# Optimization experiments

Measured on AMD Instinct MI355X. Metric: run time of the kernel, lower is better.

Reference implementation:

```python
import jax, jax.numpy as jnp
import numpy as np


def setup_inputs() -> dict:
    key = jax.random.key(0)
    k1, k2, k3, k4 = jax.random.split(key, 4)
    B, OUT, IN, K = 64, 4096, 25088, 32
    x = jax.random.normal(k1, (B, IN), dtype=jnp.float32)
    labels = jax.random.randint(k2, (OUT, IN), 0, K, dtype=jnp.int32)
    centroids = jax.random.normal(k3, (K,), dtype=jnp.float32)
    bias = jax.random.normal(k4, (OUT,), dtype=jnp.float32)
    return {"x": x, "labels": labels, "centroids": centroids, "bias": bias}


def reference(x, labels, centroids, bias):
    # Dequantize: reconstruct weight [OUT, IN] by looking labels up in the codebook
    W = centroids[labels]                      # [OUT, IN] gather
    # addmm(bias, x, W.T): [B, IN] @ [IN, OUT] + [OUT]
    return x @ W.T + bias
```

## Files before the change

### kernel.cpp

```cpp
#include <hip/hip_runtime.h>
#include <stdint.h>

typedef float f32x4 __attribute__((ext_vector_type(4)));
typedef short bf16x8 __attribute__((ext_vector_type(8)));
typedef int   i32x4  __attribute__((ext_vector_type(4)));

#define IN_DIM   25088
#define OUT_DIM  4096
#define BATCH    64
#define SPLITS   28
#define KBLK     64
#define NBLK     14
#define WG_N     128
#define LSTR     72

#define CONV_BLOCKS 784
#define INIT_BLOCKS 64

__device__ __forceinline__ uint32_t f2bf(float f) {
    uint32_t u = __builtin_bit_cast(uint32_t, f);
    return (u + 0x7FFFu + ((u >> 16) & 1u)) >> 16;
}
__device__ __forceinline__ uint32_t pack2(float a, float b) {
    return f2bf(a) | (f2bf(b) << 16);
}

__global__ __launch_bounds__(256) void prep(const float* __restrict__ x,
                                            const float* __restrict__ bias,
                                            uint32_t* __restrict__ xb,
                                            float* __restrict__ out) {
    if (blockIdx.x < CONV_BLOCKS) {
        const size_t i = blockIdx.x * 256 + threadIdx.x;
        const float4 v0 = *(const float4*)(x + i * 8);
        const float4 v1 = *(const float4*)(x + i * 8 + 4);
        uint4 o;
        o.x = pack2(v0.x, v0.y); o.y = pack2(v0.z, v0.w);
        o.z = pack2(v1.x, v1.y); o.w = pack2(v1.z, v1.w);
        *(uint4*)(xb + i * 4) = o;
    } else {
        const size_t g = (size_t)(blockIdx.x - CONV_BLOCKS) * 256 + threadIdx.x;
        const float4* b4 = (const float4*)bias;
        float4* o4 = (float4*)out;
        #pragma unroll
        for (int r = 0; r < 4; ++r) {
            const size_t j = g * 4 + r;
            o4[j] = b4[j & (OUT_DIM / 4 - 1)];
        }
    }
}

__global__ __launch_bounds__(256) void qlinear_main(
    const int*      __restrict__ labels,
    const float*    __restrict__ centroids,
    const uint16_t* __restrict__ xb,
    float*          __restrict__ out)
{
    __shared__ __align__(16) uint32_t table[1024];
    __shared__ __align__(16) uint16_t wt[WG_N * LSTR];
    __shared__ __align__(16) uint16_t xt[BATCH * LSTR];

    const int t     = threadIdx.x;
    const int wgn   = blockIdx.x & 31;
    const int split = blockIdx.x >> 5;
    const int o0    = wgn * WG_N;
    const int kbase = split * (KBLK * NBLK);

    #pragma unroll
    for (int e = 0; e < 4; ++e) {
        const int i = t + 256 * e;
        table[i] = f2bf(centroids[i & 31]) | (f2bf(centroids[i >> 5]) << 16);
    }

    const int lane = t & 63;
    const int wave = t >> 6;
    const int ln   = lane & 15;
    const int lq   = lane >> 4;

    const int srow = t >> 3;
    const int skc  = (t & 7) * 8;

    const int xrow = t >> 2;
    const int xseg = (t & 3) * 16;

    const int* lbase[4];
    #pragma unroll
    for (int p = 0; p < 4; ++p)
        lbase[p] = labels + (size_t)(o0 + p * 32 + srow) * IN_DIM + kbase + skc;

    f32x4 acc[4][2] = {};

    i32x4 pl[4][2];
    #pragma unroll
    for (int p = 0; p < 4; ++p) {
        pl[p][0] = __builtin_nontemporal_load((const i32x4*)lbase[p]);
        pl[p][1] = __builtin_nontemporal_load((const i32x4*)lbase[p] + 1);
    }

    for (int blk = 0; blk < NBLK; ++blk) {
        const int k0 = kbase + blk * KBLK;

        i32x4 npl[4][2];
        if (blk + 1 < NBLK) {
            #pragma unroll
            for (int p = 0; p < 4; ++p) {
                const i32x4* lp = (const i32x4*)(lbase[p] + (blk + 1) * KBLK);
                npl[p][0] = __builtin_nontemporal_load(lp);
                npl[p][1] = __builtin_nontemporal_load(lp + 1);
            }
        }

        __syncthreads();

        #pragma unroll
        for (int p = 0; p < 4; ++p) {
            const int row = p * 32 + srow;
            uint4 w;
            w.x = table[(uint32_t)pl[p][0].x | ((uint32_t)pl[p][0].y << 5)];
            w.y = table[(uint32_t)pl[p][0].z | ((uint32_t)pl[p][0].w << 5)];
            w.z = table[(uint32_t)pl[p][1].x | ((uint32_t)pl[p][1].y << 5)];
            w.w = table[(uint32_t)pl[p][1].z | ((uint32_t)pl[p][1].w << 5)];
            *(uint4*)(wt + row * LSTR + skc) = w;
        }
        {
            const uint16_t* xp = xb + (size_t)xrow * IN_DIM + k0 + xseg;
            const bf16x8 v0 = *(const bf16x8*)xp;
            const bf16x8 v1 = *(const bf16x8*)(xp + 8);
            *(bf16x8*)(xt + xrow * LSTR + xseg)     = v0;
            *(bf16x8*)(xt + xrow * LSTR + xseg + 8) = v1;
        }
        __syncthreads();

        #pragma unroll
        for (int ks = 0; ks < 2; ++ks) {
            const int kk = ks * 32 + lq * 8;
            bf16x8 a[4], b[2];
            #pragma unroll
            for (int mt = 0; mt < 4; ++mt)
                a[mt] = *(const bf16x8*)(xt + (mt * 16 + ln) * LSTR + kk);
            #pragma unroll
            for (int nt = 0; nt < 2; ++nt)
                b[nt] = *(const bf16x8*)(wt + (wave * 32 + nt * 16 + ln) * LSTR + kk);
            #pragma unroll
            for (int mt = 0; mt < 4; ++mt)
                #pragma unroll
                for (int nt = 0; nt < 2; ++nt)
                    acc[mt][nt] = __builtin_amdgcn_mfma_f32_16x16x32_bf16(
                        a[mt], b[nt], acc[mt][nt], 0, 0, 0);
        }

        #pragma unroll
        for (int p = 0; p < 4; ++p) {
            pl[p][0] = npl[p][0];
            pl[p][1] = npl[p][1];
        }
    }

    #pragma unroll
    for (int mt = 0; mt < 4; ++mt)
        #pragma unroll
        for (int nt = 0; nt < 2; ++nt) {
            const int o = o0 + wave * 32 + nt * 16 + ln;
            #pragma unroll
            for (int r = 0; r < 4; ++r)
                atomicAdd(out + (size_t)(mt * 16 + lq * 4 + r) * OUT_DIM + o,
                          acc[mt][nt][r]);
        }
}

extern "C" void kernel_launch(void* const* d_in, const int* in_sizes, int n_in,
                              void* d_out, int out_size, void* d_ws, size_t ws_size,
                              hipStream_t stream) {
    const float* x         = (const float*)d_in[0];
    const int*   labels    = (const int*)d_in[1];
    const float* centroids = (const float*)d_in[2];
    const float* bias      = (const float*)d_in[3];
    float* out = (float*)d_out;

    uint32_t* xb = (uint32_t*)d_ws;

    prep<<<CONV_BLOCKS + INIT_BLOCKS, 256, 0, stream>>>(x, bias, xb, out);
    qlinear_main<<<32 * SPLITS, 256, 0, stream>>>(labels, centroids,
                                                  (const uint16_t*)xb, out);
}
```

Measured before the change: 543.4 us.

## Load labels and x directly into MFMA fragment registers, dropping LDS staging

Each lane now loads the label and bf16 activation data that its MFMA fragments need straight from global memory, and decodes the weights through the shared codebook table in registers. The LDS tiles for W and x and the two barriers per k-block are removed. This cuts LDS traffic and synchronisation. In exchange, the x tile is no longer shared across waves, so each wave re-reads it from global or cache, and the label loads become less coalesced (64-byte chunks per row per lane group).

```diff
diff --git a/kernel.cpp b/kernel.cpp
--- a/kernel.cpp
+++ b/kernel.cpp
@@ -12,7 +12,6 @@
 #define KBLK     64
 #define NBLK     14
 #define WG_N     128
-#define LSTR     72
 
 #define CONV_BLOCKS 784
 #define INIT_BLOCKS 64
@@ -56,8 +55,6 @@
     float*          __restrict__ out)
 {
     __shared__ __align__(16) uint32_t table[1024];
-    __shared__ __align__(16) uint16_t wt[WG_N * LSTR];
-    __shared__ __align__(16) uint16_t xt[BATCH * LSTR];
 
     const int t     = threadIdx.x;
     const int wgn   = blockIdx.x & 31;
@@ -70,88 +67,85 @@
         const int i = t + 256 * e;
         table[i] = f2bf(centroids[i & 31]) | (f2bf(centroids[i >> 5]) << 16);
     }
+    __syncthreads();
 
     const int lane = t & 63;
     const int wave = t >> 6;
     const int ln   = lane & 15;
     const int lq   = lane >> 4;
 
-    const int srow = t >> 3;
-    const int skc  = (t & 7) * 8;
+    const int* lp0 = labels + (size_t)(o0 + wave * 32 +  0 + ln) * IN_DIM + kbase + lq * 8;
+    const int* lp1 = labels + (size_t)(o0 + wave * 32 + 16 + ln) * IN_DIM + kbase + lq * 8;
 
-    const int xrow = t >> 2;
-    const int xseg = (t & 3) * 16;
-
-    const int* lbase[4];
+    const uint16_t* xp[4];
     #pragma unroll
-    for (int p = 0; p < 4; ++p)
-        lbase[p] = labels + (size_t)(o0 + p * 32 + srow) * IN_DIM + kbase + skc;
+    for (int mt = 0; mt < 4; ++mt)
+        xp[mt] = xb + (size_t)(mt * 16 + ln) * IN_DIM + kbase + lq * 8;
 
     f32x4 acc[4][2] = {};
 
-    i32x4 pl[4][2];
+    i32x4 cur[2][2][2];
     #pragma unroll
-    for (int p = 0; p < 4; ++p) {
-        pl[p][0] = __builtin_nontemporal_load((const i32x4*)lbase[p]);
-        pl[p][1] = __builtin_nontemporal_load((const i32x4*)lbase[p] + 1);
+    for (int nt = 0; nt < 2; ++nt) {
+        const int* lp = nt ? lp1 : lp0;
+        #pragma unroll
+        for (int ks = 0; ks < 2; ++ks) {
+            const i32x4* p = (const i32x4*)(lp + ks * 32);
+            cur[nt][ks][0] = __builtin_nontemporal_load(p);
+            cur[nt][ks][1] = __builtin_nontemporal_load(p + 1);
+        }
     }
 
     for (int blk = 0; blk < NBLK; ++blk) {
-        const int k0 = kbase + blk * KBLK;
+        const int koff = blk * KBLK;
 
-        i32x4 npl[4][2];
+        bf16x8 a[2][4];
+        #pragma unroll
+        for (int ks = 0; ks < 2; ++ks)
+            #pragma unroll
+            for (int mt = 0; mt < 4; ++mt)
+                a[ks][mt] = *(const bf16x8*)(xp[mt] + koff + ks * 32);
+
+        i32x4 nxt[2][2][2];
         if (blk + 1 < NBLK) {
             #pragma unroll
-            for (int p = 0; p < 4; ++p) {
-                const i32x4* lp = (const i32x4*)(lbase[p] + (blk + 1) * KBLK);
-                npl[p][0] = __builtin_nontemporal_load(lp);
-                npl[p][1] = __builtin_nontemporal_load(lp + 1);
+            for (int nt = 0; nt < 2; ++nt) {
+                const int* lp = (nt ? lp1 : lp0) + koff + KBLK;
+                #pragma unroll
+                for (int ks = 0; ks < 2; ++ks) {
+                    const i32x4* p = (const i32x4*)(lp + ks * 32);
+                    nxt[nt][ks][0] = __builtin_nontemporal_load(p);
+                    nxt[nt][ks][1] = __builtin_nontemporal_load(p + 1);
+                }
             }
         }
 
-        __syncthreads();
-
-        #pragma unroll
-        for (int p = 0; p < 4; ++p) {
-            const int row = p * 32 + srow;
-            uint4 w;
-            w.x = table[(uint32_t)pl[p][0].x | ((uint32_t)pl[p][0].y << 5)];
-            w.y = table[(uint32_t)pl[p][0].z | ((uint32_t)pl[p][0].w << 5)];
-            w.z = table[(uint32_t)pl[p][1].x | ((uint32_t)pl[p][1].y << 5)];
-            w.w = table[(uint32_t)pl[p][1].z | ((uint32_t)pl[p][1].w << 5)];
-            *(uint4*)(wt + row * LSTR + skc) = w;
-        }
-        {
-            const uint16_t* xp = xb + (size_t)xrow * IN_DIM + k0 + xseg;
-            const bf16x8 v0 = *(const bf16x8*)xp;
-            const bf16x8 v1 = *(const bf16x8*)(xp + 8);
-            *(bf16x8*)(xt + xrow * LSTR + xseg)     = v0;
-            *(bf16x8*)(xt + xrow * LSTR + xseg + 8) = v1;
-        }
-        __syncthreads();
-
         #pragma unroll
         for (int ks = 0; ks < 2; ++ks) {
-            const int kk = ks * 32 + lq * 8;
-            bf16x8 a[4], b[2];
             #pragma unroll
-            for (int mt = 0; mt < 4; ++mt)
-                a[mt] = *(const bf16x8*)(xt + (mt * 16 + ln) * LSTR + kk);
+            for (int nt = 0; nt < 2; ++nt) {
+                union { bf16x8 v; uint32_t u[4]; } b;
+                const i32x4 v0 = cur[nt][ks][0];
+                const i32x4 v1 = cur[nt][ks][1];
+                b.u[0] = table[(uint32_t)v0.x | ((uint32_t)v0.y << 5)];
+                b.u[1] = table[(uint32_t)v0.z | ((uint32_t)v0.w << 5)];
+                b.u[2] = table[(uint32_t)v1.x | ((uint32_t)v1.y << 5)];
+                b.u[3] = table[(uint32_t)v1.z | ((uint32_t)v1.w << 5)];
+                #pragma unroll
+                for (int mt = 0; mt < 4; ++mt)
+                    acc[mt][nt] = __builtin_amdgcn_mfma_f32_16x16x32_bf16(
+                        a[ks][mt], b.v, acc[mt][nt], 0, 0, 0);
+            }
+        }
+
+        if (blk + 1 < NBLK) {
             #pragma unroll
             for (int nt = 0; nt < 2; ++nt)
-                b[nt] = *(const bf16x8*)(wt + (wave * 32 + nt * 16 + ln) * LSTR + kk);
-            #pragma unroll
-            for (int mt = 0; mt < 4; ++mt)
                 #pragma unroll
-                for (int nt = 0; nt < 2; ++nt)
-                    acc[mt][nt] = __builtin_amdgcn_mfma_f32_16x16x32_bf16(
-                        a[mt], b[nt], acc[mt][nt], 0, 0, 0);
-        }
-
-        #pragma unroll
-        for (int p = 0; p < 4; ++p) {
-            pl[p][0] = npl[p][0];
-            pl[p][1] = npl[p][1];
+                for (int ks = 0; ks < 2; ++ks) {
+                    cur[nt][ks][0] = nxt[nt][ks][0];
+                    cur[nt][ks][1] = nxt[nt][ks][1];
+                }
         }
     }
 
```

Result: slower. 599.1 us (+10.2%).
